# Kernel optimization log

Hardware: AMD Instinct MI355X
Metric: run time of the kernel (lower is better)

## Reference

```python
import jax, jax.numpy as jnp
import numpy as np

B, V, D, E, F, H, HD = 16, 1024, 16, 64, 16, 128, 64
GRAPH_LAYERS, FLOW_ITERS, DUAL_ITERS = 2, 10, 10
STEP, MOM, BIG = 0.01, 0.9, 1e9


def _build_graph():
    # circulant graph: node v's d-th out-neighbor is v + offs[d] (mod V); offsets paired (o, -o)
    offs = np.array([1, -1, 2, -2, 3, -3, 4, -4, 5, -5, 6, -6, 7, -7, 8, -8], dtype=np.int32)
    v = np.arange(V, dtype=np.int32)[:, None]
    d = np.broadcast_to(np.arange(D, dtype=np.int32)[None, :], (V, D))
    adj = ((v + offs[None, :]) % V).astype(np.int32)
    inv_adj = ((v - offs[None, :]) % V).astype(np.int32)
    in_idx = np.stack([inv_adj, d], axis=-1)    # d-th incoming edge of v == out-edge (inv_adj[v,d], slot d)
    rev_idx = np.stack([adj, d], axis=-1)       # out-edge (v,d) is the d-th incoming edge of adj[v,d]
    opp_idx = np.stack([adj, d ^ 1], axis=-1)   # opposite edge (w->v) is slot d^1 at w (paired offsets)
    bt = lambda x: jnp.asarray(np.broadcast_to(x[None], (B,) + x.shape).copy())
    return bt(adj), bt(inv_adj), bt(in_idx), bt(rev_idx), bt(opp_idx)


def setup_inputs() -> dict:
    key = jax.random.key(0)
    ks = jax.random.split(key, 16)
    adj_lst, inv_adj_lst, in_indices, rev_indices, opp_indices = _build_graph()
    rn = lambda k, shape, scale=1.0: jax.random.normal(k, shape, dtype=jnp.float32) * scale
    s = lambda fan: 1.0 / float(np.sqrt(fan))
    return {
        'demands': rn(ks[0], (B, V, 1)),
        'node_features': rn(ks[1], (B, V, F)),
        'edge_lengths': jax.random.uniform(ks[2], (B, V, D), dtype=jnp.float32),
        'norm_edge_lengths': jax.random.uniform(ks[3], (B, V, D), dtype=jnp.float32),
        'node_emb': rn(ks[4], (V, E)),
        'W_enc': rn(ks[5], (E + F, H), s(E + F)), 'b_enc': jnp.zeros((H,), jnp.float32),
        'W_gat': rn(ks[6], (H, H), s(H)), 'b_gat': jnp.zeros((H,), jnp.float32),
        'a_gat': rn(ks[7], (H,), s(H)),
        'W_gru_x': rn(ks[8], (H, 3 * H), s(H)), 'W_gru_h': rn(ks[9], (H, 3 * H), s(H)),
        'b_gru': jnp.zeros((3 * H,), jnp.float32),
        'W_dec1': rn(ks[10], (2 * H, HD), s(2 * H)), 'b_dec1': jnp.zeros((HD,), jnp.float32),
        'W_dec2': rn(ks[11], (HD, 1), s(HD)), 'b_dec2': jnp.zeros((1,), jnp.float32),
        'W_dual1': rn(ks[12], (H, HD), s(H)), 'b_dual1': jnp.zeros((HD,), jnp.float32),
        'W_dual2': rn(ks[13], (HD, 1), s(HD)), 'b_dual2': jnp.zeros((1,), jnp.float32),
        'adj_lst': adj_lst, 'inv_adj_lst': inv_adj_lst,
        'in_indices': in_indices, 'rev_indices': rev_indices, 'opp_indices': opp_indices,
        'num_nodes': jnp.full((B,), V, dtype=jnp.int32),
    }


def _gather_nodes(values, idx, valid):
    # masked_gather with set_zero=True: values (B,V,H), idx (B,V,D) -> (B,V,D,H)
    bb = jnp.arange(values.shape[0])[:, None, None]
    g = values[bb, jnp.clip(idx, 0, values.shape[1] - 1)]
    return g * valid[..., None]


def _gather_edges(x, idx):
    # gather_nd into a (B,V,D,...) tensor; idx (B,V,D,2) = (node, slot), batch implicit
    bb = jnp.arange(x.shape[0])[:, None, None]
    return x[bb, idx[..., 0], idx[..., 1]]


def _sparsemax(z):
    n = z.shape[-1]
    zs = jnp.sort(z, axis=-1)[..., ::-1]
    k = jnp.arange(1, n + 1, dtype=z.dtype)
    zc = jnp.cumsum(zs, axis=-1)
    support = (1.0 + k * zs) > zc
    kz = jnp.sum(support, axis=-1, keepdims=True)
    tau = (jnp.take_along_axis(zc, kz - 1, axis=-1) - 1.0) / kz.astype(z.dtype)
    return jnp.maximum(z - tau, 0.0)


def _forward(demands, node_features, edge_lengths, norm_edge_lengths, node_emb, W_enc, b_enc,
             W_gat, b_gat, a_gat, W_gru_x, W_gru_h, b_gru, W_dec1, b_dec1, W_dec2, b_dec2,
             W_dual1, b_dual1, W_dual2, b_dual2,
             adj_lst, inv_adj_lst, in_indices, rev_indices, opp_indices, num_nodes):
    f32 = jnp.float32
    # embedding lookup with max_norm=1
    nrm = jnp.linalg.norm(node_emb, axis=-1, keepdims=True)
    emb = node_emb / jnp.maximum(nrm, 1.0)
    emb_b = jnp.broadcast_to(emb[None], (demands.shape[0], V, E))
    node_enc = jnp.concatenate([emb_b, node_features], axis=-1) @ W_enc + b_enc   # (B,V,H)
    mask = (adj_lst == num_nodes[:, None, None]).astype(f32)                       # 1 = padded slot
    valid = 1.0 - mask
    initial = _gather_nodes(node_enc, adj_lst, valid)                              # (B,V,D,H)
    h = initial
    for _ in range(GRAPH_LAYERS):
        # DirectionalGAT: per-edge transform, masked attention over slots, directional regather
        t = jnp.tanh(h @ W_gat + b_gat)                                            # (B,V,D,H)
        logits = jnp.einsum('bvdh,h->bvd', t, a_gat) - BIG * mask
        attn = jax.nn.softmax(logits, axis=-1)
        node_msg = jnp.einsum('bvd,bvdh->bvh', attn, t)                            # (B,V,H)
        msg = _gather_nodes(node_msg, adj_lst, valid)
        x = jnp.tanh(msg + initial)
        # GRU cell, shared weights over all edge states
        gx = x @ W_gru_x + b_gru
        gh = h @ W_gru_h
        z = jax.nn.sigmoid(gx[..., :H] + gh[..., :H])
        r = jax.nn.sigmoid(gx[..., H:2 * H] + gh[..., H:2 * H])
        cand = jnp.tanh(gx[..., 2 * H:] + r * gh[..., 2 * H:])
        h = z * h + (1.0 - z) * cand
    # decoder over (encoding, encoding + opposite-edge encoding)
    comb = h + _gather_edges(h, opp_indices)
    dec_in = jnp.concatenate([h, comb], axis=-1)
    nw = (jnp.tanh(dec_in @ W_dec1 + b_dec1) @ W_dec2 + b_dec2)[..., 0]            # (B,V,D)
    # destination attention: normalize over incoming edges, map back to outgoing layout
    inv_mask = (inv_adj_lst == num_nodes[:, None, None]).astype(f32)
    in_w = _gather_edges(nw, in_indices)
    dest_attn = jax.nn.softmax(in_w - BIG * inv_mask, axis=-1)
    nw = _gather_edges(dest_attn, rev_indices)
    pred = nw - BIG * mask
    normalized = _sparsemax(pred) * valid
    # iterative proportional min-cost-flow solver
    def mcf_step(flow, _):
        inflow = jnp.sum(_gather_edges(flow, in_indices), axis=-1, keepdims=True)  # (B,V,1)
        return normalized * jax.nn.relu(inflow - demands), None
    flow, _ = jax.lax.scan(mcf_step, jnp.zeros_like(normalized), None, length=FLOW_ITERS)
    flow_cost = jnp.sum(flow * flow, axis=(1, 2))                                  # square cost fn
    # dual variables + dual flow (projected momentum gradient descent)
    node_states = jnp.sum(h, axis=2)                                               # (B,V,H)
    dual_vars = jax.nn.relu(jnp.tanh(node_states @ W_dual1 + b_dual1) @ W_dual2 + b_dual2)  # (B,V,1)
    dual = mask * dual_vars
    dual_tr = _gather_nodes(dual_vars, adj_lst, valid)[..., 0]
    dual_diff = dual_tr - dual                                                     # (B,V,D)
    def dual_step(carry, _):
        f, vel = carry
        grad = 2.0 * f + dual_diff                                                 # d/df [f^2 + dual_diff*f]
        vel = MOM * vel - STEP * grad
        f = jax.nn.relu(f + vel)
        return (f, vel), None
    (dual_flows, _), _ = jax.lax.scan(dual_step, (jnp.zeros_like(dual_diff), jnp.zeros_like(dual_diff)), None, length=DUAL_ITERS)
    dual_flows = dual_flows * valid
    dual_demand = jnp.sum(dual_vars * demands, axis=(1, 2))
    dual_cost = jnp.sum(dual_flows * dual_flows + dual_diff * dual_flows, axis=(1, 2)) - dual_demand
    return flow_cost - dual_cost                                                   # (B,) primal-dual gap loss


def reference(demands, node_features, edge_lengths, norm_edge_lengths, node_emb, W_enc, b_enc,
              W_gat, b_gat, a_gat, W_gru_x, W_gru_h, b_gru, W_dec1, b_dec1, W_dec2, b_dec2,
              W_dual1, b_dual1, W_dual2, b_dual2,
              adj_lst, inv_adj_lst, in_indices, rev_indices, opp_indices, num_nodes):
    return _forward(demands, node_features, edge_lengths, norm_edge_lengths, node_emb, W_enc, b_enc,
                    W_gat, b_gat, a_gat, W_gru_x, W_gru_h, b_gru, W_dec1, b_dec1, W_dec2, b_dec2,
                    W_dual1, b_dual1, W_dual2, b_dual2,
                    adj_lst, inv_adj_lst, in_indices, rev_indices, opp_indices, num_nodes)
```

## Files before the change

### kernel.cpp

```cpp
#include <hip/hip_runtime.h>
#include <hip/hip_bf16.h>

#define B 16
#define V 1024
#define D 16
#define E 64
#define F 16
#define H 128
#define HD 64
#define BV (B*V)
#define BVD (B*V*D)

#define OFF_HNB      0
#define OFF_NORM     (OFF_HNB + BV*H/2)
#define OFF_DV       (OFF_NORM + BVD)
#define OFF_WT       (OFF_DV + BV)
#define OFF_WTG      (OFF_WT + 65536)
#define OFF_WPQ      (OFF_WTG + 8192)
#define OFF_WU1T     (OFF_WPQ + 8192)
#define OFF_WENCT    (OFF_WU1T + 4096)

typedef __attribute__((ext_vector_type(8))) short bf16x8;
typedef __attribute__((ext_vector_type(4))) float f32x4;

__device__ __forceinline__ short f2bf(float f){
  __hip_bfloat16 b = __float2bfloat16(f);
  return *reinterpret_cast<short*>(&b);
}
__device__ __forceinline__ float bf2f(short s){
  __hip_bfloat16 b; *reinterpret_cast<short*>(&b) = s;
  return __bfloat162float(b);
}
__device__ __forceinline__ float frcp(float x){ return __builtin_amdgcn_rcpf(x); }
__device__ __forceinline__ float fsig(float x){ return frcp(1.f + __expf(-x)); }
__device__ __forceinline__ float ftanh(float x){
  float e = __expf(-2.f*fabsf(x));
  float r = (1.f - e)*frcp(1.f + e);
  return copysignf(r, x);
}

__global__ __launch_bounds__(256) void k_pre(const float* __restrict__ Wx, const float* __restrict__ Wh,
    const float* __restrict__ Wg, const float* __restrict__ W1, const float* __restrict__ Wu1,
    const float* __restrict__ Wenc,
    short* __restrict__ Wt, short* __restrict__ Wgt, short* __restrict__ Wpq,
    short* __restrict__ Wu1t, short* __restrict__ Wenct, float* __restrict__ outz){
  int bid = blockIdx.x, tid = threadIdx.x;
  if (bid == 0 && tid < 16) outz[tid] = 0.f;
  if (bid < 512){
    int n = bid, k = tid;
    int g = n >> 7, j = n & 127;
    float v;
    if (g == 0)      v = (k < 128) ? Wx[k*384 + j]       : Wh[(k-128)*384 + j];
    else if (g == 1) v = (k < 128) ? Wx[k*384 + 128 + j] : Wh[(k-128)*384 + 128 + j];
    else if (g == 2) v = (k < 128) ? Wx[k*384 + 256 + j] : 0.f;
    else             v = (k < 128) ? 0.f                 : Wh[(k-128)*384 + 256 + j];
    Wt[n*256 + k] = f2bf(v);
    return;
  }
  if (bid < 576){
    int idx = (bid-512)*256 + tid;
    int n = idx >> 7, k = idx & 127;
    Wgt[n*128 + k] = f2bf(Wg[k*128 + n]);
    return;
  }
  if (bid < 608){
    int idx = (bid-576)*256 + tid;
    int n = idx >> 7, k = idx & 127;
    float wb = W1[(k+128)*HD + n];
    float wa = W1[k*HD + n];
    Wpq[n*128 + k]      = f2bf(wa + wb);
    Wpq[(64+n)*128 + k] = f2bf(wb);
    return;
  }
  if (bid < 640){
    int idx = (bid-608)*256 + tid;
    int n = idx >> 7, k = idx & 127;
    Wu1t[n*128 + k] = f2bf(Wu1[k*HD + n]);
    return;
  }
  {
    int nn = (bid-640)*2 + (tid >> 7);
    int kk = tid & 127;
    if (kk < 96) Wenct[nn*96 + kk] = f2bf(kk < 80 ? Wenc[kk*128 + nn] : 0.f);
  }
}

__global__ __launch_bounds__(1024,4) void k_mega(const float* __restrict__ emb, const float* __restrict__ nf,
    const short* __restrict__ Wenct, const float* __restrict__ benc, const int* __restrict__ adj,
    const short* __restrict__ Wgt, const float* __restrict__ bg, const float* __restrict__ ag,
    const short* __restrict__ Wt, const float* __restrict__ bgru, short* __restrict__ hout){
  __shared__ short NE[96][136];
  __shared__ short T[96][136];
  __shared__ short H1[80][136];
  __shared__ short X[80][136];
  __shared__ float Lp[8][96];
  __shared__ float Ls[96];
  __shared__ float nrmv[96];
  short (*As)[104] = reinterpret_cast<short(*)[104]>(&H1[0][0]);

  int tid = threadIdx.x;
  int blk = blockIdx.x;
  int b = blk >> 4;
  int n0 = (blk & 15) << 6;
  int w = tid >> 6, lane = tid & 63;
  int l15 = lane & 15, quad = lane >> 4;
  int cw = w & 7, hw = w >> 3;

  if (tid < 96){
    int v = (n0 - 16 + tid) & 1023;
    const float4* e4 = reinterpret_cast<const float4*>(&emb[v*E]);
    float ss = 0.f;
    #pragma unroll
    for (int q=0;q<16;q++){ float4 x = e4[q]; ss += x.x*x.x + x.y*x.y + x.z*x.z + x.w*x.w; }
    nrmv[tid] = frcp(fmaxf(sqrtf(ss), 1.f));
  }
  __syncthreads();
  for (int e=tid; e<96*16; e+=1024){
    int r = e >> 4, q = e & 15;
    int v = (n0 - 16 + r) & 1023;
    float4 x = reinterpret_cast<const float4*>(&emb[v*E])[q];
    float iv = nrmv[r];
    short4 s; s.x=f2bf(x.x*iv); s.y=f2bf(x.y*iv); s.z=f2bf(x.z*iv); s.w=f2bf(x.w*iv);
    *reinterpret_cast<short4*>(&As[r][q*4]) = s;
  }
  for (int e=tid; e<96*4; e+=1024){
    int r = e >> 2, q = e & 3;
    int m = (b<<10) + ((n0 - 16 + r) & 1023);
    float4 x = reinterpret_cast<const float4*>(&nf[(long)m*F])[q];
    short4 s; s.x=f2bf(x.x); s.y=f2bf(x.y); s.z=f2bf(x.z); s.w=f2bf(x.w);
    *reinterpret_cast<short4*>(&As[r][64 + q*4]) = s;
    short4 z; z.x=0; z.y=0; z.z=0; z.w=0;
    *reinterpret_cast<short4*>(&As[r][80 + q*4]) = z;
  }
  __syncthreads();
  {
    f32x4 acc[3];
    #pragma unroll
    for (int t=0;t<3;t++) acc[t] = (f32x4){0.f,0.f,0.f,0.f};
    #pragma unroll
    for (int kc=0;kc<3;kc++){
      int k0 = kc*32;
      bf16x8 bfr = *reinterpret_cast<const bf16x8*>(&Wenct[(16*cw + l15)*96 + k0 + quad*8]);
      #pragma unroll
      for (int t=0;t<3;t++){
        bf16x8 a = *reinterpret_cast<const bf16x8*>(&As[16*(3*hw+t) + l15][k0 + quad*8]);
        acc[t] = __builtin_amdgcn_mfma_f32_16x16x32_bf16(a, bfr, acc[t], 0,0,0);
      }
    }
    int c = 16*cw + l15;
    float bb = benc[c];
    #pragma unroll
    for (int t=0;t<3;t++)
      #pragma unroll
      for (int reg=0;reg<4;reg++)
        NE[16*(3*hw+t) + quad*4 + reg][c] = f2bf(acc[t][reg] + bb);
  }
  __syncthreads();
  {
    f32x4 acc[3];
    #pragma unroll
    for (int t=0;t<3;t++) acc[t] = (f32x4){0.f,0.f,0.f,0.f};
    #pragma unroll
    for (int kc=0;kc<4;kc++){
      int k0 = kc*32;
      bf16x8 bfr = *reinterpret_cast<const bf16x8*>(&Wgt[(16*cw + l15)*128 + k0 + quad*8]);
      #pragma unroll
      for (int t=0;t<3;t++){
        bf16x8 a = *reinterpret_cast<const bf16x8*>(&NE[16*(3*hw+t) + l15][k0 + quad*8]);
        acc[t] = __builtin_amdgcn_mfma_f32_16x16x32_bf16(a, bfr, acc[t], 0,0,0);
      }
    }
    int c = 16*cw + l15;
    float bgc = bg[c], agc = ag[c];
    float lp[3][4];
    #pragma unroll
    for (int t=0;t<3;t++)
      #pragma unroll
      for (int reg=0;reg<4;reg++){
        float tt = ftanh(acc[t][reg] + bgc);
        T[16*(3*hw+t) + quad*4 + reg][c] = f2bf(tt);
        lp[t][reg] = tt * agc;
      }
    #pragma unroll
    for (int t=0;t<3;t++)
      #pragma unroll
      for (int reg=0;reg<4;reg++){
        lp[t][reg] += __shfl_xor(lp[t][reg], 1);
        lp[t][reg] += __shfl_xor(lp[t][reg], 2);
        lp[t][reg] += __shfl_xor(lp[t][reg], 4);
        lp[t][reg] += __shfl_xor(lp[t][reg], 8);
      }
    if (l15 == 0){
      #pragma unroll
      for (int t=0;t<3;t++)
        #pragma unroll
        for (int reg=0;reg<4;reg++)
          Lp[cw][16*(3*hw+t) + quad*4 + reg] = lp[t][reg];
    }
  }
  __syncthreads();
  if (tid < 96){
    float s = 0.f;
    #pragma unroll
    for (int i=0;i<8;i++) s += Lp[i][tid];
    Ls[tid] = s;
  }
  __syncthreads();
  if (tid < 640){
    int vl = tid >> 3, seg = tid & 7;
    int wg = (b<<10) + ((n0 - 8 + vl) & 1023);
    int li[16]; float at[16];
    float m = -1e30f;
    #pragma unroll
    for (int d=0; d<16; d++){
      int a = adj[wg*16 + d];
      li[d] = (a - n0 + 16) & 1023;
      m = fmaxf(m, Ls[li[d]]);
    }
    float s = 0.f;
    #pragma unroll
    for (int d=0; d<16; d++){ at[d] = __expf(Ls[li[d]] - m); s += at[d]; }
    float inv = frcp(s);
    #pragma unroll
    for (int d=0; d<16; d++) at[d] *= inv;
    #pragma unroll
    for (int c8=0; c8<2; c8++){
      int c = seg*16 + c8*8;
      float acc8[8] = {0,0,0,0,0,0,0,0};
      #pragma unroll 4
      for (int d=0; d<16; d++){
        bf16x8 tv = *reinterpret_cast<const bf16x8*>(&T[li[d]][c]);
        float a = at[d];
        #pragma unroll
        for (int q=0;q<8;q++) acc8[q] += a * bf2f(tv[q]);
      }
      bf16x8 nv = *reinterpret_cast<const bf16x8*>(&NE[vl + 8][c]);
      bf16x8 xv;
      #pragma unroll
      for (int q=0;q<8;q++) xv[q] = f2bf(ftanh(acc8[q] + bf2f(nv[q])));
      *reinterpret_cast<bf16x8*>(&X[vl][c]) = xv;
    }
  }
  __syncthreads();
  {
    f32x4 acc[3][4];
    #pragma unroll
    for (int t=0;t<3;t++)
      #pragma unroll
      for (int g=0;g<4;g++) acc[t][g] = (f32x4){0.f,0.f,0.f,0.f};
    int ncol = 16*cw + l15;
    for (int k8=0;k8<4;k8++){
      int k0 = k8*32;
      int koff = k0 + quad*8;
      bf16x8 bz = *reinterpret_cast<const bf16x8*>(&Wt[(ncol      )*256 + koff]);
      bf16x8 br = *reinterpret_cast<const bf16x8*>(&Wt[(ncol + 128)*256 + koff]);
      bf16x8 bc = *reinterpret_cast<const bf16x8*>(&Wt[(ncol + 256)*256 + koff]);
      #pragma unroll
      for (int t=0;t<3;t++){
        int mt = 3*hw + t;
        if (mt < 5){
          bf16x8 a = *reinterpret_cast<const bf16x8*>(&X[16*mt + l15][k0 + quad*8]);
          acc[t][0] = __builtin_amdgcn_mfma_f32_16x16x32_bf16(a, bz, acc[t][0], 0,0,0);
          acc[t][1] = __builtin_amdgcn_mfma_f32_16x16x32_bf16(a, br, acc[t][1], 0,0,0);
          acc[t][2] = __builtin_amdgcn_mfma_f32_16x16x32_bf16(a, bc, acc[t][2], 0,0,0);
        }
      }
    }
    for (int k8=4;k8<8;k8++){
      int k0 = k8*32;
      int koff = k0 + quad*8;
      bf16x8 bz = *reinterpret_cast<const bf16x8*>(&Wt[(ncol      )*256 + koff]);
      bf16x8 br = *reinterpret_cast<const bf16x8*>(&Wt[(ncol + 128)*256 + koff]);
      bf16x8 bc = *reinterpret_cast<const bf16x8*>(&Wt[(ncol + 384)*256 + koff]);
      #pragma unroll
      for (int t=0;t<3;t++){
        int mt = 3*hw + t;
        if (mt < 5){
          bf16x8 a = *reinterpret_cast<const bf16x8*>(&NE[16*mt + l15 + 8][k0 - 128 + quad*8]);
          acc[t][0] = __builtin_amdgcn_mfma_f32_16x16x32_bf16(a, bz, acc[t][0], 0,0,0);
          acc[t][1] = __builtin_amdgcn_mfma_f32_16x16x32_bf16(a, br, acc[t][1], 0,0,0);
          acc[t][3] = __builtin_amdgcn_mfma_f32_16x16x32_bf16(a, bc, acc[t][3], 0,0,0);
        }
      }
    }
    int j = ncol;
    float bjz = bgru[j], bjr = bgru[128 + j], bjc = bgru[256 + j];
    #pragma unroll
    for (int t=0;t<3;t++){
      int mt = 3*hw + t;
      if (mt < 5){
        #pragma unroll
        for (int reg=0;reg<4;reg++){
          int rl = 16*mt + quad*4 + reg;
          float z = fsig(acc[t][0][reg] + bjz);
          float r = fsig(acc[t][1][reg] + bjr);
          float cand = ftanh(acc[t][2][reg] + bjc + r*acc[t][3][reg]);
          float ho = bf2f(NE[rl + 8][j]);
          H1[rl][j] = f2bf(z*ho + (1.f - z)*cand);
        }
      }
    }
  }
  __syncthreads();
  {
    f32x4 acc[3];
    #pragma unroll
    for (int t=0;t<3;t++) acc[t] = (f32x4){0.f,0.f,0.f,0.f};
    #pragma unroll
    for (int kc=0;kc<4;kc++){
      int k0 = kc*32;
      bf16x8 bfr = *reinterpret_cast<const bf16x8*>(&Wgt[(16*cw + l15)*128 + k0 + quad*8]);
      #pragma unroll
      for (int t=0;t<3;t++){
        int mt = 3*hw + t;
        if (mt < 5){
          bf16x8 a = *reinterpret_cast<const bf16x8*>(&H1[16*mt + l15][k0 + quad*8]);
          acc[t] = __builtin_amdgcn_mfma_f32_16x16x32_bf16(a, bfr, acc[t], 0,0,0);
        }
      }
    }
    int c = 16*cw + l15;
    float bgc = bg[c], agc = ag[c];
    float lp[3][4];
    #pragma unroll
    for (int t=0;t<3;t++){
      int mt = 3*hw + t;
      if (mt < 5){
        #pragma unroll
        for (int reg=0;reg<4;reg++){
          float tt = ftanh(acc[t][reg] + bgc);
          T[16*mt + quad*4 + reg][c] = f2bf(tt);
          lp[t][reg] = tt * agc;
        }
      } else {
        #pragma unroll
        for (int reg=0;reg<4;reg++) lp[t][reg] = 0.f;
      }
    }
    #pragma unroll
    for (int t=0;t<3;t++)
      #pragma unroll
      for (int reg=0;reg<4;reg++){
        lp[t][reg] += __shfl_xor(lp[t][reg], 1);
        lp[t][reg] += __shfl_xor(lp[t][reg], 2);
        lp[t][reg] += __shfl_xor(lp[t][reg], 4);
        lp[t][reg] += __shfl_xor(lp[t][reg], 8);
      }
    if (l15 == 0){
      #pragma unroll
      for (int t=0;t<3;t++){
        int mt = 3*hw + t;
        if (mt < 5){
          #pragma unroll
          for (int reg=0;reg<4;reg++)
            Lp[cw][16*mt + quad*4 + reg] = lp[t][reg];
        }
      }
    }
  }
  __syncthreads();
  if (tid < 80){
    float s = 0.f;
    #pragma unroll
    for (int i=0;i<8;i++) s += Lp[i][tid];
    Ls[tid] = s;
  }
  __syncthreads();
  {
    int vl = tid >> 4, seg = tid & 15;
    int vg = (b<<10) + n0 + vl;
    int li[16]; float at[16];
    float m = -1e30f;
    #pragma unroll
    for (int d=0; d<16; d++){
      int a = adj[vg*16 + d];
      li[d] = (a - n0 + 8) & 1023;
      m = fmaxf(m, Ls[li[d]]);
    }
    float s = 0.f;
    #pragma unroll
    for (int d=0; d<16; d++){ at[d] = __expf(Ls[li[d]] - m); s += at[d]; }
    float inv = frcp(s);
    #pragma unroll
    for (int d=0; d<16; d++) at[d] *= inv;
    int c = seg*8;
    float acc8[8] = {0,0,0,0,0,0,0,0};
    #pragma unroll 4
    for (int d=0; d<16; d++){
      bf16x8 tv = *reinterpret_cast<const bf16x8*>(&T[li[d]][c]);
      float a = at[d];
      #pragma unroll
      for (int q=0;q<8;q++) acc8[q] += a * bf2f(tv[q]);
    }
    bf16x8 nv = *reinterpret_cast<const bf16x8*>(&NE[vl + 16][c]);
    bf16x8 xv;
    #pragma unroll
    for (int q=0;q<8;q++) xv[q] = f2bf(ftanh(acc8[q] + bf2f(nv[q])));
    *reinterpret_cast<bf16x8*>(&X[vl][c]) = xv;
  }
  __syncthreads();
  {
    f32x4 acc[2][4];
    #pragma unroll
    for (int t=0;t<2;t++)
      #pragma unroll
      for (int g=0;g<4;g++) acc[t][g] = (f32x4){0.f,0.f,0.f,0.f};
    int ncol = 16*cw + l15;
    for (int k8=0;k8<4;k8++){
      int k0 = k8*32;
      int koff = k0 + quad*8;
      bf16x8 bz = *reinterpret_cast<const bf16x8*>(&Wt[(ncol      )*256 + koff]);
      bf16x8 br = *reinterpret_cast<const bf16x8*>(&Wt[(ncol + 128)*256 + koff]);
      bf16x8 bc = *reinterpret_cast<const bf16x8*>(&Wt[(ncol + 256)*256 + koff]);
      #pragma unroll
      for (int t=0;t<2;t++){
        int mt = 2*hw + t;
        bf16x8 a = *reinterpret_cast<const bf16x8*>(&X[16*mt + l15][k0 + quad*8]);
        acc[t][0] = __builtin_amdgcn_mfma_f32_16x16x32_bf16(a, bz, acc[t][0], 0,0,0);
        acc[t][1] = __builtin_amdgcn_mfma_f32_16x16x32_bf16(a, br, acc[t][1], 0,0,0);
        acc[t][2] = __builtin_amdgcn_mfma_f32_16x16x32_bf16(a, bc, acc[t][2], 0,0,0);
      }
    }
    for (int k8=4;k8<8;k8++){
      int k0 = k8*32;
      int koff = k0 + quad*8;
      bf16x8 bz = *reinterpret_cast<const bf16x8*>(&Wt[(ncol      )*256 + koff]);
      bf16x8 br = *reinterpret_cast<const bf16x8*>(&Wt[(ncol + 128)*256 + koff]);
      bf16x8 bc = *reinterpret_cast<const bf16x8*>(&Wt[(ncol + 384)*256 + koff]);
      #pragma unroll
      for (int t=0;t<2;t++){
        int mt = 2*hw + t;
        bf16x8 a = *reinterpret_cast<const bf16x8*>(&H1[16*mt + l15 + 8][k0 - 128 + quad*8]);
        acc[t][0] = __builtin_amdgcn_mfma_f32_16x16x32_bf16(a, bz, acc[t][0], 0,0,0);
        acc[t][1] = __builtin_amdgcn_mfma_f32_16x16x32_bf16(a, br, acc[t][1], 0,0,0);
        acc[t][3] = __builtin_amdgcn_mfma_f32_16x16x32_bf16(a, bc, acc[t][3], 0,0,0);
      }
    }
    __syncthreads();
    int j = ncol;
    float bjz = bgru[j], bjr = bgru[128 + j], bjc = bgru[256 + j];
    #pragma unroll
    for (int t=0;t<2;t++){
      int mt = 2*hw + t;
      #pragma unroll
      for (int reg=0;reg<4;reg++){
        int rl = 16*mt + quad*4 + reg;
        float z = fsig(acc[t][0][reg] + bjz);
        float r = fsig(acc[t][1][reg] + bjr);
        float cand = ftanh(acc[t][2][reg] + bjc + r*acc[t][3][reg]);
        float ho = bf2f(H1[rl + 8][j]);
        X[rl][j] = f2bf(z*ho + (1.f - z)*cand);
      }
    }
  }
  __syncthreads();
  for (int idx=tid; idx<64*16; idx+=1024){
    int r = idx >> 4, c8 = idx & 15;
    *reinterpret_cast<bf16x8*>(&hout[(long)((b<<10) + n0 + r)*128 + c8*8]) =
        *reinterpret_cast<const bf16x8*>(&X[r][c8*8]);
  }
}

__global__ __launch_bounds__(1024,4) void k_decdas(const short* __restrict__ hn, const int* __restrict__ adj,
    const int* __restrict__ invadj, const short* __restrict__ Wpq, const float* __restrict__ b1,
    const float* __restrict__ W2, const float* __restrict__ b2_,
    const short* __restrict__ Wu1t, const float* __restrict__ bu1, const float* __restrict__ Wu2,
    const float* __restrict__ bu2_, float* __restrict__ norm_, float* __restrict__ dv){
  __shared__ short Hs[112][136];
  __shared__ short PQb[112][132];
  __shared__ short NSs[64][136];
  __shared__ int adjL[64][16];
  __shared__ float dvp[64][4];
  __shared__ float b1s[64], w2s[64], bu1s[64], wu2s[64];
  int tid = threadIdx.x;
  int blk = blockIdx.x;
  int b = blk >> 4;
  int n0 = (blk & 15) << 6;
  if (tid < 64){ b1s[tid] = b1[tid]; w2s[tid] = W2[tid]; bu1s[tid] = bu1[tid]; wu2s[tid] = Wu2[tid]; }
  for (int idx=tid; idx<112*16; idx+=1024){
    int r = idx >> 4, c8 = idx & 15;
    int g = (b << 10) + ((n0 - 24 + r) & 1023);
    *reinterpret_cast<bf16x8*>(&Hs[r][c8*8]) =
        *reinterpret_cast<const bf16x8*>(&hn[(long)g*128 + c8*8]);
  }
  {
    int r = tid >> 4, d = tid & 15;
    int a = adj[((b<<10) + n0 + r)*16 + d];
    adjL[r][d] = (a - n0 + 24) & 1023;
  }
  __syncthreads();
  int w = tid >> 6, lane = tid & 63;
  int l15 = lane & 15, quad = lane >> 4;
  int cw = w & 7, hw = w >> 3;
  {
    f32x4 acc[4];
    #pragma unroll
    for (int t=0;t<4;t++) acc[t] = (f32x4){0.f,0.f,0.f,0.f};
    #pragma unroll
    for (int kc=0;kc<4;kc++){
      int k0 = kc*32;
      bf16x8 bfr = *reinterpret_cast<const bf16x8*>(&Wpq[(16*cw + l15)*128 + k0 + quad*8]);
      #pragma unroll
      for (int t=0;t<4;t++){
        int mt = 4*hw + t;
        if (mt < 7){
          bf16x8 a = *reinterpret_cast<const bf16x8*>(&Hs[16*mt + l15][k0 + quad*8]);
          acc[t] = __builtin_amdgcn_mfma_f32_16x16x32_bf16(a, bfr, acc[t], 0,0,0);
        }
      }
    }
    int c = 16*cw + l15;
    #pragma unroll
    for (int t=0;t<4;t++){
      int mt = 4*hw + t;
      if (mt < 7){
        #pragma unroll
        for (int reg=0;reg<4;reg++)
          PQb[16*mt + quad*4 + reg][c] = f2bf(acc[t][reg]);
      }
    }
  }
  {
    int r = tid >> 4, c8 = tid & 15;
    float acc8[8] = {0,0,0,0,0,0,0,0};
    #pragma unroll 4
    for (int d=0; d<16; d++){
      bf16x8 hv = *reinterpret_cast<const bf16x8*>(&Hs[adjL[r][d]][c8*8]);
      #pragma unroll
      for (int q=0;q<8;q++) acc8[q] += bf2f(hv[q]);
    }
    bf16x8 sv;
    #pragma unroll
    for (int q=0;q<8;q++) sv[q] = f2bf(acc8[q]);
    *reinterpret_cast<bf16x8*>(&NSs[r][c8*8]) = sv;
  }
  __syncthreads();
  if (w < 8){
    int c4 = w & 3, h2 = w >> 2;
    f32x4 acc[2];
    #pragma unroll
    for (int t=0;t<2;t++) acc[t] = (f32x4){0.f,0.f,0.f,0.f};
    #pragma unroll
    for (int kc=0;kc<4;kc++){
      int k0 = kc*32;
      bf16x8 bfr = *reinterpret_cast<const bf16x8*>(&Wu1t[(16*c4 + l15)*128 + k0 + quad*8]);
      #pragma unroll
      for (int t=0;t<2;t++){
        bf16x8 a = *reinterpret_cast<const bf16x8*>(&NSs[16*(2*h2+t) + l15][k0 + quad*8]);
        acc[t] = __builtin_amdgcn_mfma_f32_16x16x32_bf16(a, bfr, acc[t], 0,0,0);
      }
    }
    int n = 16*c4 + l15;
    float bn = bu1s[n], wn = wu2s[n];
    #pragma unroll
    for (int t=0;t<2;t++){
      #pragma unroll
      for (int reg=0;reg<4;reg++){
        float p = ftanh(acc[t][reg] + bn) * wn;
        p += __shfl_xor(p, 1);
        p += __shfl_xor(p, 2);
        p += __shfl_xor(p, 4);
        p += __shfl_xor(p, 8);
        if (l15 == 0) dvp[16*(2*h2+t) + quad*4 + reg][c4] = p;
      }
    }
  }
  __syncthreads();
  float* nws = reinterpret_cast<float*>(&Hs[0][0]);
  float b2v = b2_[0];
  for (int e = tid; e < 96*16; e += 1024){
    int rr = e >> 4, d = e & 15;
    int wnode = (n0 + rr - 16) & 1023;
    int wg = (b<<10) + wnode;
    int a = adj[wg*16 + d];
    int al = (a - n0 + 24) & 1023;
    int wl = rr + 8;
    float p = 0.f;
    #pragma unroll 8
    for (int c=0;c<64;c++)
      p += ftanh(bf2f(PQb[al][c]) + bf2f(PQb[wl][64 + c]) + b1s[c]) * w2s[c];
    nws[rr*17 + d] = p + b2v;
  }
  __syncthreads();
  if (tid < 64){
    float val = dvp[tid][0]+dvp[tid][1]+dvp[tid][2]+dvp[tid][3];
    dv[(b<<10) + n0 + tid] = fmaxf(val + bu2_[0], 0.f);
  }
  float* datt = reinterpret_cast<float*>(&PQb[0][0]);
  if (tid < 80){
    int wnode = (n0 + tid - 8) & 1023;
    int wg = (b<<10) + wnode;
    float vals[16];
    float m = -1e30f;
    #pragma unroll
    for (int d=0; d<16; d++){
      int iv = invadj[wg*16 + d];
      int il = (iv - n0 + 16) & 1023;
      vals[d] = nws[il*17 + d];
      m = fmaxf(m, vals[d]);
    }
    float s = 0.f;
    #pragma unroll
    for (int d=0; d<16; d++){ vals[d] = __expf(vals[d]-m); s += vals[d]; }
    float inv = frcp(s);
    #pragma unroll
    for (int d=0; d<16; d++) datt[tid*17 + d] = vals[d]*inv;
  }
  __syncthreads();
  if (tid < 64){
    int vg = (b<<10) + n0 + tid;
    float z[16], s[16];
    #pragma unroll
    for (int d=0; d<16; d++){
      int al = adjL[tid][d] - 16;
      z[d] = datt[al*17 + d];
      s[d] = z[d];
    }
    #pragma unroll
    for (int k2 = 2; k2 <= 16; k2 <<= 1){
      #pragma unroll
      for (int jj = k2 >> 1; jj > 0; jj >>= 1){
        #pragma unroll
        for (int i = 0; i < 16; i++){
          int l = i ^ jj;
          if (l > i){
            bool up = ((i & k2) == 0);
            float a = s[i], bb = s[l];
            bool sw = up ? (a > bb) : (a < bb);
            if (sw){ s[i]=bb; s[l]=a; }
          }
        }
      }
    }
    float cs = 0.f, zcs = 0.f; int kz = 1;
    #pragma unroll
    for (int j=0;j<16;j++){
      float zj = s[15-j];
      cs += zj;
      if (1.f + (float)(j+1)*zj > cs){ kz = j+1; zcs = cs; }
    }
    float tau = (zcs - 1.f)/(float)kz;
    #pragma unroll
    for (int d=0; d<16; d++) norm_[(long)vg*16 + d] = fmaxf(z[d]-tau, 0.f);
  }
}

__global__ __launch_bounds__(256) void k_flowfin(const float* __restrict__ norm_,
    const float* __restrict__ dem, const int* __restrict__ invadj, const float* __restrict__ dv,
    float* __restrict__ out){
  __shared__ float nrmS[224*17];
  __shared__ float sbuf[2][224];
  __shared__ float red[4];
  int tid = threadIdx.x;
  int blk = blockIdx.x;
  int b = blk >> 4;
  int t0 = (blk & 15) << 6;
  for (int e=tid; e<224*4; e+=256){
    int r = e >> 2, q4 = e & 3;
    int v = (t0 - 80 + r) & 1023;
    float4 x = reinterpret_cast<const float4*>(&norm_[(long)((b<<10) + v)*16])[q4];
    nrmS[r*17 + q4*4+0] = x.x; nrmS[r*17 + q4*4+1] = x.y;
    nrmS[r*17 + q4*4+2] = x.z; nrmS[r*17 + q4*4+3] = x.w;
  }
  bool act = tid < 224;
  int r = tid;
  float dm = 0.f; int gv = 0;
  int ivl[16];
  if (act){
    int v = (t0 - 80 + r) & 1023;
    gv = (b<<10) + v;
    dm = dem[gv];
    #pragma unroll
    for (int d4=0; d4<4; d4++){
      int4 i4 = reinterpret_cast<const int4*>(&invadj[(long)gv*16])[d4];
      int t;
      t = (i4.x - t0 + 80) & 1023; ivl[d4*4+0] = t < 224 ? t : 223;
      t = (i4.y - t0 + 80) & 1023; ivl[d4*4+1] = t < 224 ? t : 223;
      t = (i4.z - t0 + 80) & 1023; ivl[d4*4+2] = t < 224 ? t : 223;
      t = (i4.w - t0 + 80) & 1023; ivl[d4*4+3] = t < 224 ? t : 223;
    }
    sbuf[0][r] = 0.f;
  }
  __syncthreads();
  float nrg[16];
  if (act){
    #pragma unroll
    for (int d=0; d<16; d++) nrg[d] = nrmS[ivl[d]*17 + d];
  }
  int p = 0;
  float s = 0.f;
  for (int it=0; it<10; it++){
    if (act){
      float inflow = 0.f;
      #pragma unroll
      for (int d=0; d<16; d++) inflow += nrg[d]*sbuf[p][ivl[d]];
      s = fmaxf(inflow - dm, 0.f);
      sbuf[1-p][r] = s;
    }
    p ^= 1;
    __syncthreads();
  }
  float partF = 0.f, partD = 0.f, partDD = 0.f;
  if (act && r >= 80 && r < 144){
    float nr2 = 0.f;
    #pragma unroll
    for (int d=0; d<16; d++){ float nv = nrmS[r*17 + d]; nr2 += nv*nv; }
    partF = nr2 * s * s;
    float dvv = dv[gv];
    float f = 0.f, vel = 0.f;
    #pragma unroll
    for (int it=0; it<10; it++){
      float g = 2.f*f + dvv;
      vel = 0.9f*vel - 0.01f*g;
      f = fmaxf(f + vel, 0.f);
    }
    partD = f*f + dvv*f;
    partDD = dvv * dm;
  }
  float val = partF - 16.f*partD + partDD;
  #pragma unroll
  for (int off=32; off>0; off>>=1) val += __shfl_down(val, off);
  if ((tid & 63) == 0) red[tid>>6] = val;
  __syncthreads();
  if (tid == 0) atomicAdd(&out[b], red[0]+red[1]+red[2]+red[3]);
}

extern "C" void kernel_launch(void* const* d_in, const int* in_sizes, int n_in,
                              void* d_out, int out_size, void* d_ws, size_t ws_size,
                              hipStream_t stream){
  (void)in_sizes; (void)n_in; (void)out_size; (void)ws_size;
  const float* demands = (const float*)d_in[0];
  const float* nf      = (const float*)d_in[1];
  const float* emb     = (const float*)d_in[4];
  const float* Wenc    = (const float*)d_in[5];
  const float* benc    = (const float*)d_in[6];
  const float* Wgat    = (const float*)d_in[7];
  const float* bgat    = (const float*)d_in[8];
  const float* agat    = (const float*)d_in[9];
  const float* Wgx     = (const float*)d_in[10];
  const float* Wgh     = (const float*)d_in[11];
  const float* bgru    = (const float*)d_in[12];
  const float* Wd1     = (const float*)d_in[13];
  const float* bd1     = (const float*)d_in[14];
  const float* Wd2     = (const float*)d_in[15];
  const float* bd2     = (const float*)d_in[16];
  const float* Wu1     = (const float*)d_in[17];
  const float* bu1     = (const float*)d_in[18];
  const float* Wu2     = (const float*)d_in[19];
  const float* bu2     = (const float*)d_in[20];
  const int* adj       = (const int*)d_in[21];
  const int* invadj    = (const int*)d_in[22];

  float* ws    = (float*)d_ws;
  short* hnB   = (short*)(ws + OFF_HNB);
  float* nrm   = ws + OFF_NORM;
  float* dv    = ws + OFF_DV;
  short* wt    = (short*)(ws + OFF_WT);
  short* wtg   = (short*)(ws + OFF_WTG);
  short* wpq   = (short*)(ws + OFF_WPQ);
  short* wu1t  = (short*)(ws + OFF_WU1T);
  short* wenct = (short*)(ws + OFF_WENCT);

  k_pre<<<704, 256, 0, stream>>>(Wgx, Wgh, Wgat, Wd1, Wu1, Wenc, wt, wtg, wpq, wu1t, wenct,
                                 (float*)d_out);
  k_mega<<<BV/64, 1024, 0, stream>>>(emb, nf, wenct, benc, adj, wtg, bgat, agat, wt, bgru, hnB);
  k_decdas<<<BV/64, 1024, 0, stream>>>(hnB, adj, invadj, wpq, bd1, Wd2, bd2,
                                       wu1t, bu1, Wu2, bu2, nrm, dv);
  k_flowfin<<<B*16, 256, 0, stream>>>(nrm, demands, invadj, dv, (float*)d_out);
}
```

Before: 203.3 us.

## Replace GAT neighbor aggregation with dense attention-matrix MFMA over transposed T

The per-thread gather-and-FMA attention aggregation in both GAT layers becomes a dense banded attention matrix A2 in shared memory, multiplied against a transposed tanh tile Tt using bf16 MFMA. This moves neighbor accumulation from scalar FMAs to matrix cores and hoists the adjacency loads into registers reused by both layers. The embedding-norm computation is also spread across four threads per row. The matrix is mostly zeros, so the added zero-fill, extra LDS, dropped min-occupancy launch bound, and bf16 rounding of attention weights are the tradeoffs.

```diff
diff --git a/kernel.cpp b/kernel.cpp
--- a/kernel.cpp
+++ b/kernel.cpp
@@ -85,14 +85,15 @@
   }
 }
 
-__global__ __launch_bounds__(1024,4) void k_mega(const float* __restrict__ emb, const float* __restrict__ nf,
+__global__ __launch_bounds__(1024) void k_mega(const float* __restrict__ emb, const float* __restrict__ nf,
     const short* __restrict__ Wenct, const float* __restrict__ benc, const int* __restrict__ adj,
     const short* __restrict__ Wgt, const float* __restrict__ bg, const float* __restrict__ ag,
     const short* __restrict__ Wt, const float* __restrict__ bgru, short* __restrict__ hout){
   __shared__ short NE[96][136];
-  __shared__ short T[96][136];
+  __shared__ short Tt[128][104];
   __shared__ short H1[80][136];
   __shared__ short X[80][136];
+  __shared__ short A2[80][104];
   __shared__ float Lp[8][96];
   __shared__ float Ls[96];
   __shared__ float nrmv[96];
@@ -106,13 +107,30 @@
   int l15 = lane & 15, quad = lane >> 4;
   int cw = w & 7, hw = w >> 3;
 
-  if (tid < 96){
-    int v = (n0 - 16 + tid) & 1023;
+  int li96[16];
+  if (tid < 80){
+    int wg = (b<<10) + ((n0 - 8 + tid) & 1023);
+    const int4* a4 = reinterpret_cast<const int4*>(&adj[(long)wg*16]);
+    #pragma unroll
+    for (int d4=0; d4<4; d4++){
+      int4 i4 = a4[d4];
+      li96[d4*4+0] = (i4.x - n0 + 16) & 1023;
+      li96[d4*4+1] = (i4.y - n0 + 16) & 1023;
+      li96[d4*4+2] = (i4.z - n0 + 16) & 1023;
+      li96[d4*4+3] = (i4.w - n0 + 16) & 1023;
+    }
+  }
+
+  if (tid < 384){
+    int r = tid >> 2, q = tid & 3;
+    int v = (n0 - 16 + r) & 1023;
     const float4* e4 = reinterpret_cast<const float4*>(&emb[v*E]);
     float ss = 0.f;
     #pragma unroll
-    for (int q=0;q<16;q++){ float4 x = e4[q]; ss += x.x*x.x + x.y*x.y + x.z*x.z + x.w*x.w; }
-    nrmv[tid] = frcp(fmaxf(sqrtf(ss), 1.f));
+    for (int qq=0;qq<4;qq++){ float4 x = e4[q*4+qq]; ss += x.x*x.x + x.y*x.y + x.z*x.z + x.w*x.w; }
+    ss += __shfl_xor(ss, 1);
+    ss += __shfl_xor(ss, 2);
+    if (q == 0) nrmv[r] = frcp(fmaxf(sqrtf(ss), 1.f));
   }
   __syncthreads();
   for (int e=tid; e<96*16; e+=1024){
@@ -174,13 +192,16 @@
     float bgc = bg[c], agc = ag[c];
     float lp[3][4];
     #pragma unroll
-    for (int t=0;t<3;t++)
+    for (int t=0;t<3;t++){
+      short4 tv;
       #pragma unroll
       for (int reg=0;reg<4;reg++){
         float tt = ftanh(acc[t][reg] + bgc);
-        T[16*(3*hw+t) + quad*4 + reg][c] = f2bf(tt);
+        reinterpret_cast<short*>(&tv)[reg] = f2bf(tt);
         lp[t][reg] = tt * agc;
       }
+      *reinterpret_cast<short4*>(&Tt[c][16*(3*hw+t) + quad*4]) = tv;
+    }
     #pragma unroll
     for (int t=0;t<3;t++)
       #pragma unroll
@@ -205,40 +226,55 @@
     for (int i=0;i<8;i++) s += Lp[i][tid];
     Ls[tid] = s;
   }
-  __syncthreads();
-  if (tid < 640){
-    int vl = tid >> 3, seg = tid & 7;
-    int wg = (b<<10) + ((n0 - 8 + vl) & 1023);
-    int li[16]; float at[16];
+  if (tid < 960){
+    bf16x8 z8;
+    #pragma unroll
+    for (int q=0;q<8;q++) z8[q] = 0;
+    int r = tid/12, c8 = tid%12;
+    *reinterpret_cast<bf16x8*>(&A2[r][c8*8]) = z8;
+  }
+  __syncthreads();
+  if (tid < 80){
+    float at[16];
     float m = -1e30f;
     #pragma unroll
-    for (int d=0; d<16; d++){
-      int a = adj[wg*16 + d];
-      li[d] = (a - n0 + 16) & 1023;
-      m = fmaxf(m, Ls[li[d]]);
-    }
+    for (int d=0; d<16; d++) m = fmaxf(m, Ls[li96[d]]);
     float s = 0.f;
     #pragma unroll
-    for (int d=0; d<16; d++){ at[d] = __expf(Ls[li[d]] - m); s += at[d]; }
+    for (int d=0; d<16; d++){ at[d] = __expf(Ls[li96[d]] - m); s += at[d]; }
     float inv = frcp(s);
     #pragma unroll
-    for (int d=0; d<16; d++) at[d] *= inv;
-    #pragma unroll
-    for (int c8=0; c8<2; c8++){
-      int c = seg*16 + c8*8;
-      float acc8[8] = {0,0,0,0,0,0,0,0};
-      #pragma unroll 4
-      for (int d=0; d<16; d++){
-        bf16x8 tv = *reinterpret_cast<const bf16x8*>(&T[li[d]][c]);
-        float a = at[d];
+    for (int d=0; d<16; d++) A2[tid][li96[d]] = f2bf(at[d]*inv);
+  }
+  __syncthreads();
+  {
+    f32x4 acc[3];
+    #pragma unroll
+    for (int t=0;t<3;t++) acc[t] = (f32x4){0.f,0.f,0.f,0.f};
+    #pragma unroll
+    for (int kc=0;kc<3;kc++){
+      int k0 = kc*32;
+      bf16x8 bfr = *reinterpret_cast<const bf16x8*>(&Tt[16*cw + l15][k0 + quad*8]);
+      #pragma unroll
+      for (int t=0;t<3;t++){
+        int mt = 3*hw + t;
+        if (mt < 5){
+          bf16x8 a = *reinterpret_cast<const bf16x8*>(&A2[16*mt + l15][k0 + quad*8]);
+          acc[t] = __builtin_amdgcn_mfma_f32_16x16x32_bf16(a, bfr, acc[t], 0,0,0);
+        }
+      }
+    }
+    int c = 16*cw + l15;
+    #pragma unroll
+    for (int t=0;t<3;t++){
+      int mt = 3*hw + t;
+      if (mt < 5){
         #pragma unroll
-        for (int q=0;q<8;q++) acc8[q] += a * bf2f(tv[q]);
-      }
-      bf16x8 nv = *reinterpret_cast<const bf16x8*>(&NE[vl + 8][c]);
-      bf16x8 xv;
-      #pragma unroll
-      for (int q=0;q<8;q++) xv[q] = f2bf(ftanh(acc8[q] + bf2f(nv[q])));
-      *reinterpret_cast<bf16x8*>(&X[vl][c]) = xv;
+        for (int reg=0;reg<4;reg++){
+          int rl = 16*mt + quad*4 + reg;
+          X[rl][c] = f2bf(ftanh(acc[t][reg] + bf2f(NE[rl + 8][c])));
+        }
+      }
     }
   }
   __syncthreads();
@@ -326,12 +362,14 @@
     for (int t=0;t<3;t++){
       int mt = 3*hw + t;
       if (mt < 5){
+        short4 tv;
         #pragma unroll
         for (int reg=0;reg<4;reg++){
           float tt = ftanh(acc[t][reg] + bgc);
-          T[16*mt + quad*4 + reg][c] = f2bf(tt);
+          reinterpret_cast<short*>(&tv)[reg] = f2bf(tt);
           lp[t][reg] = tt * agc;
         }
+        *reinterpret_cast<short4*>(&Tt[c][16*mt + quad*4]) = tv;
       } else {
         #pragma unroll
         for (int reg=0;reg<4;reg++) lp[t][reg] = 0.f;
@@ -365,38 +403,50 @@
     for (int i=0;i<8;i++) s += Lp[i][tid];
     Ls[tid] = s;
   }
-  __syncthreads();
-  {
-    int vl = tid >> 4, seg = tid & 15;
-    int vg = (b<<10) + n0 + vl;
-    int li[16]; float at[16];
+  if (tid < 768){
+    bf16x8 z8;
+    #pragma unroll
+    for (int q=0;q<8;q++) z8[q] = 0;
+    int r = tid/12, c8 = tid%12;
+    *reinterpret_cast<bf16x8*>(&A2[r][c8*8]) = z8;
+  }
+  __syncthreads();
+  if (tid >= 8 && tid < 72){
+    int r5 = tid - 8;
+    float at[16];
     float m = -1e30f;
     #pragma unroll
-    for (int d=0; d<16; d++){
-      int a = adj[vg*16 + d];
-      li[d] = (a - n0 + 8) & 1023;
-      m = fmaxf(m, Ls[li[d]]);
-    }
+    for (int d=0; d<16; d++) m = fmaxf(m, Ls[li96[d] - 8]);
     float s = 0.f;
     #pragma unroll
-    for (int d=0; d<16; d++){ at[d] = __expf(Ls[li[d]] - m); s += at[d]; }
+    for (int d=0; d<16; d++){ at[d] = __expf(Ls[li96[d] - 8] - m); s += at[d]; }
     float inv = frcp(s);
     #pragma unroll
-    for (int d=0; d<16; d++) at[d] *= inv;
-    int c = seg*8;
-    float acc8[8] = {0,0,0,0,0,0,0,0};
-    #pragma unroll 4
-    for (int d=0; d<16; d++){
-      bf16x8 tv = *reinterpret_cast<const bf16x8*>(&T[li[d]][c]);
-      float a = at[d];
-      #pragma unroll
-      for (int q=0;q<8;q++) acc8[q] += a * bf2f(tv[q]);
-    }
-    bf16x8 nv = *reinterpret_cast<const bf16x8*>(&NE[vl + 16][c]);
-    bf16x8 xv;
-    #pragma unroll
-    for (int q=0;q<8;q++) xv[q] = f2bf(ftanh(acc8[q] + bf2f(nv[q])));
-    *reinterpret_cast<bf16x8*>(&X[vl][c]) = xv;
+    for (int d=0; d<16; d++) A2[r5][li96[d] - 8] = f2bf(at[d]*inv);
+  }
+  __syncthreads();
+  {
+    f32x4 acc[2];
+    #pragma unroll
+    for (int t=0;t<2;t++) acc[t] = (f32x4){0.f,0.f,0.f,0.f};
+    #pragma unroll
+    for (int kc=0;kc<3;kc++){
+      int k0 = kc*32;
+      bf16x8 bfr = *reinterpret_cast<const bf16x8*>(&Tt[16*cw + l15][k0 + quad*8]);
+      #pragma unroll
+      for (int t=0;t<2;t++){
+        bf16x8 a = *reinterpret_cast<const bf16x8*>(&A2[16*(2*hw+t) + l15][k0 + quad*8]);
+        acc[t] = __builtin_amdgcn_mfma_f32_16x16x32_bf16(a, bfr, acc[t], 0,0,0);
+      }
+    }
+    int c = 16*cw + l15;
+    #pragma unroll
+    for (int t=0;t<2;t++)
+      #pragma unroll
+      for (int reg=0;reg<4;reg++){
+        int rl = 16*(2*hw+t) + quad*4 + reg;
+        X[rl][c] = f2bf(ftanh(acc[t][reg] + bf2f(NE[rl + 16][c])));
+      }
   }
   __syncthreads();
   {
@@ -454,8 +504,8 @@
     }
   }
   __syncthreads();
-  for (int idx=tid; idx<64*16; idx+=1024){
-    int r = idx >> 4, c8 = idx & 15;
+  if (tid < 64*16){
+    int r = tid >> 4, c8 = tid & 15;
     *reinterpret_cast<bf16x8*>(&hout[(long)((b<<10) + n0 + r)*128 + c8*8]) =
         *reinterpret_cast<const bf16x8*>(&X[r][c8*8]);
   }
```

Result: faster. 186.3 us (-8.3%).
